# Kernel optimization log

Hardware: AMD Instinct MI355X
Metric: run time of the kernel (lower is better)

## Reference

```python
import jax, jax.numpy as jnp
import numpy as np

DIM = 256
NUM_HEADS = 8
HEAD_DIM = DIM // NUM_HEADS


def setup_inputs() -> dict:
    key = jax.random.key(0)
    k_x, k_wq, k_bq, k_wp, k_bp = jax.random.split(key, 5)
    B, C, H, W = 2, DIM, 48, 48
    x = jax.random.normal(k_x, (B, C, H, W), dtype=jnp.float32)
    # 1x1 convs are pointwise matmuls: store weights as [out, in]
    w_qkv = jax.random.normal(k_wq, (3 * C, C), dtype=jnp.float32) * (1.0 / np.sqrt(C))
    b_qkv = jax.random.normal(k_bq, (3 * C,), dtype=jnp.float32) * 0.01
    w_proj = jax.random.normal(k_wp, (C, C), dtype=jnp.float32) * (1.0 / np.sqrt(C))
    b_proj = jax.random.normal(k_bp, (C,), dtype=jnp.float32) * 0.01
    return {"x": x, "w_qkv": w_qkv, "b_qkv": b_qkv, "w_proj": w_proj, "b_proj": b_proj}


def reference(x, w_qkv, b_qkv, w_proj, b_proj):
    B, C, H, W = x.shape
    N = H * W
    # qkv 1x1 conv -> pointwise channel matmul
    qkv = jnp.einsum('bchw,oc->bohw', x, w_qkv) + b_qkv[None, :, None, None]
    q, k, v = jnp.split(qkv, 3, axis=1)  # each [B, C, H, W]
    q = q.reshape(B, NUM_HEADS, HEAD_DIM, N)
    k = k.reshape(B, NUM_HEADS, HEAD_DIM, N)
    v = v.reshape(B, NUM_HEADS, HEAD_DIM, N)
    scale = 1.0 / (HEAD_DIM ** 0.5)
    attn = jnp.einsum('bhdn,bhdm->bhnm', q, k) * scale  # [B, H, N, N]
    attn = jax.nn.softmax(attn, axis=-1)
    out = jnp.einsum('bhnm,bhdm->bhdn', attn, v)  # [B, heads, head_dim, N]
    out = out.reshape(B, C, H, W)
    out = jnp.einsum('bchw,oc->bohw', out, w_proj) + b_proj[None, :, None, None]
    return out + x
```

## Files before the change

### kernel.cpp

```cpp
#include <hip/hip_runtime.h>
#include <math.h>

#define C_DIM 256
#define NH 8
#define HD 32
#define BATCH 2
#define NPIX 2304
#define TK 64
#define NGRP (NPIX / 16)
#define TPB 36

typedef __attribute__((ext_vector_type(8))) short bf16x8;
typedef __attribute__((ext_vector_type(4))) float f32x4;

#define OFF_XT  0u
#define OFF_Q   1179648u
#define OFF_K   2359296u
#define OFF_V   3538944u
#define OFF_OT  4718592u
#define OFF_WQ  5898240u
#define OFF_WP  6094848u

__device__ __forceinline__ unsigned short f2b(float f) {
    union { float f; unsigned int u; } c; c.f = f;
    unsigned int u = c.u + 0x7FFFu + ((c.u >> 16) & 1u);
    return (unsigned short)(u >> 16);
}
__device__ __forceinline__ unsigned int pk2(float lo, float hi) {
    union { float f; unsigned int u; } a, b;
    a.f = lo; b.f = hi;
    return __builtin_amdgcn_perm(b.u + 0x8000u, a.u + 0x8000u, 0x07060302u);
}
__device__ __forceinline__ unsigned int cvtpk(float lo, float hi) {
    unsigned int r;
    asm("v_cvt_pk_bf16_f32 %0, %1, %2" : "=v"(r) : "v"(lo), "v"(hi));
    return r;
}
__device__ __forceinline__ float fexp2(float x) {
#if __has_builtin(__builtin_amdgcn_exp2f)
    return __builtin_amdgcn_exp2f(x);
#else
    return exp2f(x);
#endif
}

__global__ __launch_bounds__(256) void prep_all(
        const float* __restrict__ x, unsigned short* __restrict__ xT,
        const float* __restrict__ wqkv, const float* __restrict__ wproj,
        unsigned short* __restrict__ wq, unsigned short* __restrict__ wp)
{
    __shared__ unsigned short t_s[64][72];
    const int bid = blockIdx.x;
    const int tid = threadIdx.x;
    if (bid < 288) {
        const int bx = bid % 36, by = (bid / 36) & 3, bz = bid / 144;
        const int n0 = bx * 64, c0 = by * 64, b = bz;
        const int nl = tid & 63, cq = tid >> 6;
        #pragma unroll
        for (int p = 0; p < 8; ++p) {
            const int c = p * 8 + cq * 2;
            const float f0 = x[((size_t)b * C_DIM + c0 + c) * NPIX + n0 + nl];
            const float f1 = x[((size_t)b * C_DIM + c0 + c + 1) * NPIX + n0 + nl];
            *(unsigned int*)&t_s[nl][c] = pk2(f0, f1);
        }
        __syncthreads();
        const int row = tid >> 2, jq = tid & 3;
        #pragma unroll
        for (int hh = 0; hh < 2; ++hh) {
            const int jl = jq * 2 + hh;
            const int jg = by * 8 + jl;
            const int ngrp = bx * 4 + (row >> 4);
            unsigned short* dst = xT + (((size_t)b * NGRP + ngrp) * 32 + jg) * 128 + (row & 15) * 8;
            *(uint4*)dst = *(uint4*)&t_s[row][jl * 8];
        }
    } else {
        const int t = (bid - 288) * 256 + tid;
        const float* src; unsigned short* dst;
        if (t < 24576) {
            const int m = t >> 5, j = t & 31;
            src = wqkv + ((size_t)m * C_DIM + j * 8);
            dst = wq + ((size_t)((m >> 4) * 32 + j) * 16 + (m & 15)) * 8;
        } else {
            const int t2 = t - 24576, m = t2 >> 5, j = t2 & 31;
            src = wproj + ((size_t)m * C_DIM + j * 8);
            dst = wp + ((size_t)((m >> 4) * 32 + j) * 16 + (m & 15)) * 8;
        }
        const float4 f0 = *(const float4*)src, f1 = *(const float4*)(src + 4);
        *(uint4*)dst = make_uint4(pk2(f0.x, f0.y), pk2(f0.z, f0.w),
                                  pk2(f1.x, f1.y), pk2(f1.z, f1.w));
    }
}

__global__ __launch_bounds__(256, 2) void qkv_gemm(
        const unsigned short* __restrict__ xT, const unsigned short* __restrict__ wq,
        const float* __restrict__ bias,
        unsigned short* __restrict__ Qg, unsigned short* __restrict__ Kg,
        unsigned short* __restrict__ Vg)
{
    __shared__ unsigned short eplds[4][2560];
    const int tid = threadIdx.x, wv = tid >> 6, lane = tid & 63;
    const int l15 = lane & 15, quad = lane >> 4;
    const int n0 = blockIdx.x * 256, my = blockIdx.y, b = blockIdx.z;
    const int nw = n0 + wv * 64;

    bf16x8 af[2][8];
    #pragma unroll
    for (int mt = 0; mt < 2; ++mt)
        #pragma unroll
        for (int kc = 0; kc < 8; ++kc)
            af[mt][kc] = *(const bf16x8*)(wq +
                ((size_t)((my * 2 + mt) * 32 + kc * 4 + quad) * 16 + l15) * 8);

    f32x4 acc[2][4];
    #pragma unroll
    for (int mt = 0; mt < 2; ++mt)
        #pragma unroll
        for (int s = 0; s < 4; ++s) acc[mt][s] = (f32x4){0.f, 0.f, 0.f, 0.f};

    #pragma unroll
    for (int sub = 0; sub < 4; ++sub) {
        const int ngrp = (nw + sub * 16) >> 4;
        const unsigned short* bp = xT + ((size_t)b * NGRP + ngrp) * 32 * 128;
        #pragma unroll
        for (int kc = 0; kc < 8; ++kc) {
            const bf16x8 bf = *(const bf16x8*)(bp + (size_t)(kc * 4 + quad) * 128 + l15 * 8);
            acc[0][sub] = __builtin_amdgcn_mfma_f32_16x16x32_bf16(af[0][kc], bf, acc[0][sub], 0, 0, 0);
            acc[1][sub] = __builtin_amdgcn_mfma_f32_16x16x32_bf16(af[1][kc], bf, acc[1][sub], 0, 0, 0);
        }
    }

    const int which = my >> 3;
    const int h = my & 7, bh = b * NH + h;
    float4 b4[2];
    b4[0] = *(const float4*)(bias + my * 32 + quad * 4);
    b4[1] = *(const float4*)(bias + my * 32 + 16 + quad * 4);
    unsigned short* wl = eplds[wv];

    if (which < 2) {
        const float sc = (which == 0) ? 0.2550348576f : 1.0f;
        #pragma unroll
        for (int mt = 0; mt < 2; ++mt)
            #pragma unroll
            for (int sub = 0; sub < 4; ++sub) {
                const float v0 = (acc[mt][sub][0] + b4[mt].x) * sc;
                const float v1 = (acc[mt][sub][1] + b4[mt].y) * sc;
                const float v2 = (acc[mt][sub][2] + b4[mt].z) * sc;
                const float v3 = (acc[mt][sub][3] + b4[mt].w) * sc;
                *(uint2*)&wl[(sub * 16 + l15) * 40 + mt * 16 + quad * 4] =
                    make_uint2(pk2(v0, v1), pk2(v2, v3));
            }
        unsigned short* dst = ((which == 0) ? Qg : Kg)
                            + ((size_t)bh * NPIX + nw + lane) * HD;
        #pragma unroll
        for (int i = 0; i < 4; ++i)
            *((uint4*)dst + i) = *(uint4*)&wl[lane * 40 + i * 8];
    } else {
        #pragma unroll
        for (int mt = 0; mt < 2; ++mt)
            #pragma unroll
            for (int sub = 0; sub < 4; ++sub) {
                wl[(mt * 16 + quad * 4 + 0) * 72 + sub * 16 + l15] = f2b(acc[mt][sub][0] + b4[mt].x);
                wl[(mt * 16 + quad * 4 + 1) * 72 + sub * 16 + l15] = f2b(acc[mt][sub][1] + b4[mt].y);
                wl[(mt * 16 + quad * 4 + 2) * 72 + sub * 16 + l15] = f2b(acc[mt][sub][2] + b4[mt].z);
                wl[(mt * 16 + quad * 4 + 3) * 72 + sub * 16 + l15] = f2b(acc[mt][sub][3] + b4[mt].w);
            }
        const int row = lane >> 1, seg = (lane & 1) * 32;
        unsigned short* dst = Vg + ((size_t)bh * HD + row) * NPIX + nw + seg;
        #pragma unroll
        for (int i = 0; i < 4; ++i)
            *((uint4*)dst + i) = *(uint4*)&wl[row * 72 + seg + i * 8];
    }
}

__global__ __launch_bounds__(256, 4) void attn_kernel(
        const unsigned short* __restrict__ Qg, const unsigned short* __restrict__ Kg,
        const unsigned short* __restrict__ Vg,
        unsigned short* __restrict__ OtT)
{
    __shared__ unsigned short k_s[2][TK][40];
    __shared__ unsigned short v_s[2][HD][76];

    const int tid  = threadIdx.x;
    const int wv   = tid >> 6;
    const int lane = tid & 63;
    const int l15  = lane & 15;
    const int quad = lane >> 4;
    const int bh   = blockIdx.x;
    const int q0   = blockIdx.y * 64;

    const unsigned short* Qh = Qg + (size_t)bh * NPIX * HD;
    const unsigned short* Kh = Kg + (size_t)bh * NPIX * HD;
    const unsigned short* Vh = Vg + (size_t)bh * HD * NPIX;

    const bf16x8 q_frag = *(const bf16x8*)(Qh + (size_t)(q0 + wv * 16 + l15) * HD + quad * 8);
    const bf16x8 onesf = {16256, 16256, 16256, 16256, 16256, 16256, 16256, 16256};

    const int kr = tid >> 2, kc = (tid & 3) * 8;
    const int ksl = (kr & 0x23) | ((kr & 0x04) << 2) | ((kr & 0x18) >> 1);
    const int vd = tid >> 3, vc = (tid & 7) * 8;

    uint4 kreg = *(const uint4*)(Kh + (size_t)kr * HD + kc);
    uint4 vreg = *(const uint4*)(Vh + (size_t)vd * NPIX + vc);
    *(uint4*)&k_s[0][ksl][kc] = kreg;
    *(uint4*)&v_s[0][vd][vc] = vreg;

    f32x4 o0 = {0.f, 0.f, 0.f, 0.f};
    f32x4 o1 = {0.f, 0.f, 0.f, 0.f};
    f32x4 ol = {0.f, 0.f, 0.f, 0.f};

    for (int t = 0; t < TPB; ++t) {
        const int cur = t & 1;
        if (t + 1 < TPB) {
            const int k0 = (t + 1) * TK;
            kreg = *(const uint4*)(Kh + (size_t)(k0 + kr) * HD + kc);
            vreg = *(const uint4*)(Vh + (size_t)vd * NPIX + k0 + vc);
        }
        __syncthreads();

        f32x4 s[4];
        #pragma unroll
        for (int kg = 0; kg < 4; ++kg) {
            const bf16x8 kf = *(const bf16x8*)&k_s[cur][kg * 16 + l15][quad * 8];
            s[kg] = __builtin_amdgcn_mfma_f32_16x16x32_bf16(kf, q_frag,
                        (f32x4){0.f, 0.f, 0.f, 0.f}, 0, 0, 0);
        }

        bf16x8 pf[2];
        #pragma unroll
        for (int kc2 = 0; kc2 < 2; ++kc2) {
            union { unsigned int u[4]; bf16x8 v; } c;
            c.u[0] = cvtpk(fexp2(s[2 * kc2][0]),     fexp2(s[2 * kc2][1]));
            c.u[1] = cvtpk(fexp2(s[2 * kc2][2]),     fexp2(s[2 * kc2][3]));
            c.u[2] = cvtpk(fexp2(s[2 * kc2 + 1][0]), fexp2(s[2 * kc2 + 1][1]));
            c.u[3] = cvtpk(fexp2(s[2 * kc2 + 1][2]), fexp2(s[2 * kc2 + 1][3]));
            pf[kc2] = c.v;
        }

        #pragma unroll
        for (int kc2 = 0; kc2 < 2; ++kc2) {
            const bf16x8 vf0 = *(const bf16x8*)&v_s[cur][l15][kc2 * 32 + quad * 8];
            const bf16x8 vf1 = *(const bf16x8*)&v_s[cur][16 + l15][kc2 * 32 + quad * 8];
            o0 = __builtin_amdgcn_mfma_f32_16x16x32_bf16(vf0, pf[kc2], o0, 0, 0, 0);
            o1 = __builtin_amdgcn_mfma_f32_16x16x32_bf16(vf1, pf[kc2], o1, 0, 0, 0);
            ol = __builtin_amdgcn_mfma_f32_16x16x32_bf16(onesf, pf[kc2], ol, 0, 0, 0);
        }

        if (t + 1 < TPB) {
            *(uint4*)&k_s[cur ^ 1][ksl][kc] = kreg;
            *(uint4*)&v_s[cur ^ 1][vd][vc] = vreg;
        }
    }

    const float inv = 1.f / ol[0];
    const int b = bh >> 3, h = bh & 7;
    const int qg = q0 + wv * 16 + l15;
    unsigned short* base = OtT + (((size_t)b * NGRP + (qg >> 4)) * 32 + h * 4) * 128
                         + (qg & 15) * 8;
    const int jq0 = quad >> 1, half = (quad & 1) * 4;
    const uint2 w0 = make_uint2(cvtpk(o0[0] * inv, o0[1] * inv),
                                cvtpk(o0[2] * inv, o0[3] * inv));
    const uint2 w1 = make_uint2(cvtpk(o1[0] * inv, o1[1] * inv),
                                cvtpk(o1[2] * inv, o1[3] * inv));
    *(uint2*)(base + (size_t)jq0 * 128 + half)       = w0;
    *(uint2*)(base + (size_t)(2 + jq0) * 128 + half) = w1;
}

__global__ __launch_bounds__(256) void proj_gemm(
        const unsigned short* __restrict__ OtT, const unsigned short* __restrict__ wp,
        const float* __restrict__ bias, const float* __restrict__ x,
        float* __restrict__ out)
{
    __shared__ float plds[4][576];
    const int tid = threadIdx.x, wv = tid >> 6, lane = tid & 63;
    const int l15 = lane & 15, quad = lane >> 4;
    const int n0 = blockIdx.x * 128, my = blockIdx.y, b = blockIdx.z;
    const int nw = n0 + wv * 32;

    bf16x8 af[8];
    #pragma unroll
    for (int kc = 0; kc < 8; ++kc)
        af[kc] = *(const bf16x8*)(wp + ((size_t)(my * 32 + kc * 4 + quad) * 16 + l15) * 8);

    f32x4 acc[2];
    acc[0] = (f32x4){0.f, 0.f, 0.f, 0.f};
    acc[1] = (f32x4){0.f, 0.f, 0.f, 0.f};

    #pragma unroll
    for (int sub = 0; sub < 2; ++sub) {
        const int ngrp = (nw + sub * 16) >> 4;
        const unsigned short* bp = OtT + ((size_t)b * NGRP + ngrp) * 32 * 128;
        #pragma unroll
        for (int kc = 0; kc < 8; ++kc) {
            const bf16x8 bf = *(const bf16x8*)(bp + (size_t)(kc * 4 + quad) * 128 + l15 * 8);
            acc[sub] = __builtin_amdgcn_mfma_f32_16x16x32_bf16(af[kc], bf, acc[sub], 0, 0, 0);
        }
    }

    float* wl = plds[wv];
    #pragma unroll
    for (int sub = 0; sub < 2; ++sub) {
        wl[(quad * 4 + 0) * 36 + sub * 16 + l15] = acc[sub][0];
        wl[(quad * 4 + 1) * 36 + sub * 16 + l15] = acc[sub][1];
        wl[(quad * 4 + 2) * 36 + sub * 16 + l15] = acc[sub][2];
        wl[(quad * 4 + 3) * 36 + sub * 16 + l15] = acc[sub][3];
    }
    const int m0 = my * 16;
    #pragma unroll
    for (int p = 0; p < 2; ++p) {
        const int row = p * 8 + (lane >> 3), cn = (lane & 7) * 4;
        const int c = m0 + row;
        const size_t idx = ((size_t)b * C_DIM + c) * NPIX + nw + cn;
        const f32x4 v = *(const f32x4*)&wl[row * 36 + cn];
        const f32x4 r = *(const f32x4*)(x + idx);
        const float bv = bias[c];
        f32x4 o;
        o[0] = v[0] + bv + r[0]; o[1] = v[1] + bv + r[1];
        o[2] = v[2] + bv + r[2]; o[3] = v[3] + bv + r[3];
        *(f32x4*)(out + idx) = o;
    }
}

extern "C" void kernel_launch(void* const* d_in, const int* in_sizes, int n_in,
                              void* d_out, int out_size, void* d_ws, size_t ws_size,
                              hipStream_t stream)
{
    const float* x      = (const float*)d_in[0];
    const float* w_qkv  = (const float*)d_in[1];
    const float* b_qkv  = (const float*)d_in[2];
    const float* w_proj = (const float*)d_in[3];
    const float* b_proj = (const float*)d_in[4];
    float* out = (float*)d_out;

    unsigned short* ws = (unsigned short*)d_ws;
    unsigned short* xT  = ws + OFF_XT;
    unsigned short* Qg  = ws + OFF_Q;
    unsigned short* Kg  = ws + OFF_K;
    unsigned short* Vg  = ws + OFF_V;
    unsigned short* OtT = ws + OFF_OT;
    unsigned short* wq  = ws + OFF_WQ;
    unsigned short* wp  = ws + OFF_WP;

    prep_all<<<dim3(416), 256, 0, stream>>>(x, xT, w_qkv, w_proj, wq, wp);
    qkv_gemm<<<dim3(9, 24, 2), 256, 0, stream>>>(xT, wq, b_qkv, Qg, Kg, Vg);
    attn_kernel<<<dim3(16, 36), 256, 0, stream>>>(Qg, Kg, Vg, OtT);
    proj_gemm<<<dim3(18, 16, 2), 256, 0, stream>>>(OtT, wp, b_proj, x, out);
}
```

Baseline: 105.9 us.

## Fuse four kernels into one persistent kernel with global atomic barriers

Merges prep, QKV GEMM, attention and projection into one 576-block kernel, with a software grid barrier between stages built on an atomic counter and sleep-polling. A memset clears the counters on every call. The goal is to remove three kernel launch gaps and tail bubbles. The cost is barrier overhead and stages forced onto a fixed 576-block grid. Correctness depends on all blocks being co-resident, and the bounded spin guard could let a block through early if some blocks are not yet resident.

```diff
diff --git a/kernel.cpp b/kernel.cpp
--- a/kernel.cpp
+++ b/kernel.cpp
@@ -9,6 +9,7 @@
 #define TK 64
 #define NGRP (NPIX / 16)
 #define TPB 36
+#define NBLK 576
 
 typedef __attribute__((ext_vector_type(8))) short bf16x8;
 typedef __attribute__((ext_vector_type(4))) float f32x4;
@@ -20,6 +21,7 @@
 #define OFF_OT  4718592u
 #define OFF_WQ  5898240u
 #define OFF_WP  6094848u
+#define OFF_BAR 6160384u
 
 __device__ __forceinline__ unsigned short f2b(float f) {
     union { float f; unsigned int u; } c; c.f = f;
@@ -44,17 +46,40 @@
 #endif
 }
 
-__global__ __launch_bounds__(256) void prep_all(
+__device__ __forceinline__ void gbar(unsigned int* cnt) {
+    __syncthreads();
+    if (threadIdx.x == 0) {
+        __threadfence();
+        atomicAdd(cnt, 1u);
+        int guard = 0;
+        while (__hip_atomic_load(cnt, __ATOMIC_RELAXED, __HIP_MEMORY_SCOPE_AGENT)
+                   < (unsigned)NBLK && guard < (1 << 20)) {
+            __builtin_amdgcn_s_sleep(8);
+            ++guard;
+        }
+    }
+    __syncthreads();
+    __threadfence();
+}
+
+__global__ __launch_bounds__(256, 3) void fused_pipeline(
         const float* __restrict__ x, unsigned short* __restrict__ xT,
         const float* __restrict__ wqkv, const float* __restrict__ wproj,
-        unsigned short* __restrict__ wq, unsigned short* __restrict__ wp)
+        unsigned short* __restrict__ wq, unsigned short* __restrict__ wp,
+        const float* __restrict__ bqkv,
+        unsigned short* __restrict__ Qg, unsigned short* __restrict__ Kg,
+        unsigned short* __restrict__ Vg, unsigned short* __restrict__ OtT,
+        const float* __restrict__ bproj, float* __restrict__ out,
+        unsigned int* __restrict__ bar)
 {
-    __shared__ unsigned short t_s[64][72];
+    __shared__ __align__(16) unsigned char smem[20480];
     const int bid = blockIdx.x;
     const int tid = threadIdx.x;
+
     if (bid < 288) {
-        const int bx = bid % 36, by = (bid / 36) & 3, bz = bid / 144;
-        const int n0 = bx * 64, c0 = by * 64, b = bz;
+        unsigned short (*t_s)[72] = reinterpret_cast<unsigned short(*)[72]>(smem);
+        const int bx = bid % 36, by = (bid / 36) & 3, b = bid / 144;
+        const int n0 = bx * 64, c0 = by * 64;
         const int nl = tid & 63, cq = tid >> 6;
         #pragma unroll
         for (int p = 0; p < 8; ++p) {
@@ -73,7 +98,7 @@
             unsigned short* dst = xT + (((size_t)b * NGRP + ngrp) * 32 + jg) * 128 + (row & 15) * 8;
             *(uint4*)dst = *(uint4*)&t_s[row][jl * 8];
         }
-    } else {
+    } else if (bid < 416) {
         const int t = (bid - 288) * 256 + tid;
         const float* src; unsigned short* dst;
         if (t < 24576) {
@@ -89,234 +114,221 @@
         *(uint4*)dst = make_uint4(pk2(f0.x, f0.y), pk2(f0.z, f0.w),
                                   pk2(f1.x, f1.y), pk2(f1.z, f1.w));
     }
-}
-
-__global__ __launch_bounds__(256, 2) void qkv_gemm(
-        const unsigned short* __restrict__ xT, const unsigned short* __restrict__ wq,
-        const float* __restrict__ bias,
-        unsigned short* __restrict__ Qg, unsigned short* __restrict__ Kg,
-        unsigned short* __restrict__ Vg)
-{
-    __shared__ unsigned short eplds[4][2560];
-    const int tid = threadIdx.x, wv = tid >> 6, lane = tid & 63;
-    const int l15 = lane & 15, quad = lane >> 4;
-    const int n0 = blockIdx.x * 256, my = blockIdx.y, b = blockIdx.z;
-    const int nw = n0 + wv * 64;
-
-    bf16x8 af[2][8];
-    #pragma unroll
-    for (int mt = 0; mt < 2; ++mt)
+    gbar(bar + 0);
+
+    if (bid < 432) {
+        const int wv = tid >> 6, lane = tid & 63;
+        const int l15 = lane & 15, quad = lane >> 4;
+        const int bx = bid % 9, my = (bid / 9) % 24, b = bid / 216;
+        const int n0 = bx * 256;
+        const int nw = n0 + wv * 64;
+
+        bf16x8 af[2][8];
+        #pragma unroll
+        for (int mt = 0; mt < 2; ++mt)
+            #pragma unroll
+            for (int kc = 0; kc < 8; ++kc)
+                af[mt][kc] = *(const bf16x8*)(wq +
+                    ((size_t)((my * 2 + mt) * 32 + kc * 4 + quad) * 16 + l15) * 8);
+
+        f32x4 acc[2][4];
+        #pragma unroll
+        for (int mt = 0; mt < 2; ++mt)
+            #pragma unroll
+            for (int s = 0; s < 4; ++s) acc[mt][s] = (f32x4){0.f, 0.f, 0.f, 0.f};
+
+        #pragma unroll
+        for (int sub = 0; sub < 4; ++sub) {
+            const int ngrp = (nw + sub * 16) >> 4;
+            const unsigned short* bp = xT + ((size_t)b * NGRP + ngrp) * 32 * 128;
+            #pragma unroll
+            for (int kc = 0; kc < 8; ++kc) {
+                const bf16x8 bf = *(const bf16x8*)(bp + (size_t)(kc * 4 + quad) * 128 + l15 * 8);
+                acc[0][sub] = __builtin_amdgcn_mfma_f32_16x16x32_bf16(af[0][kc], bf, acc[0][sub], 0, 0, 0);
+                acc[1][sub] = __builtin_amdgcn_mfma_f32_16x16x32_bf16(af[1][kc], bf, acc[1][sub], 0, 0, 0);
+            }
+        }
+
+        const int which = my >> 3;
+        const int h = my & 7, bh = b * NH + h;
+        float4 b4[2];
+        b4[0] = *(const float4*)(bqkv + my * 32 + quad * 4);
+        b4[1] = *(const float4*)(bqkv + my * 32 + 16 + quad * 4);
+        unsigned short* wl = (unsigned short*)smem + wv * 2560;
+
+        if (which < 2) {
+            const float sc = (which == 0) ? 0.2550348576f : 1.0f;
+            #pragma unroll
+            for (int mt = 0; mt < 2; ++mt)
+                #pragma unroll
+                for (int sub = 0; sub < 4; ++sub) {
+                    const float v0 = (acc[mt][sub][0] + b4[mt].x) * sc;
+                    const float v1 = (acc[mt][sub][1] + b4[mt].y) * sc;
+                    const float v2 = (acc[mt][sub][2] + b4[mt].z) * sc;
+                    const float v3 = (acc[mt][sub][3] + b4[mt].w) * sc;
+                    *(uint2*)&wl[(sub * 16 + l15) * 40 + mt * 16 + quad * 4] =
+                        make_uint2(pk2(v0, v1), pk2(v2, v3));
+                }
+            unsigned short* dst = ((which == 0) ? Qg : Kg)
+                                + ((size_t)bh * NPIX + nw + lane) * HD;
+            #pragma unroll
+            for (int i = 0; i < 4; ++i)
+                *((uint4*)dst + i) = *(uint4*)&wl[lane * 40 + i * 8];
+        } else {
+            #pragma unroll
+            for (int mt = 0; mt < 2; ++mt)
+                #pragma unroll
+                for (int sub = 0; sub < 4; ++sub) {
+                    wl[(mt * 16 + quad * 4 + 0) * 72 + sub * 16 + l15] = f2b(acc[mt][sub][0] + b4[mt].x);
+                    wl[(mt * 16 + quad * 4 + 1) * 72 + sub * 16 + l15] = f2b(acc[mt][sub][1] + b4[mt].y);
+                    wl[(mt * 16 + quad * 4 + 2) * 72 + sub * 16 + l15] = f2b(acc[mt][sub][2] + b4[mt].z);
+                    wl[(mt * 16 + quad * 4 + 3) * 72 + sub * 16 + l15] = f2b(acc[mt][sub][3] + b4[mt].w);
+                }
+            const int row = lane >> 1, seg = (lane & 1) * 32;
+            unsigned short* dst = Vg + ((size_t)bh * HD + row) * NPIX + nw + seg;
+            #pragma unroll
+            for (int i = 0; i < 4; ++i)
+                *((uint4*)dst + i) = *(uint4*)&wl[row * 72 + seg + i * 8];
+        }
+    }
+    gbar(bar + 1);
+
+    {
+        unsigned short* ksb = (unsigned short*)smem;
+        unsigned short* vsb = (unsigned short*)smem + 5120;
+
+        const int wv = tid >> 6, lane = tid & 63;
+        const int l15 = lane & 15, quad = lane >> 4;
+        const int bh = bid & 15;
+        const int q0 = (bid >> 4) * 64;
+
+        const unsigned short* Qh = Qg + (size_t)bh * NPIX * HD;
+        const unsigned short* Kh = Kg + (size_t)bh * NPIX * HD;
+        const unsigned short* Vh = Vg + (size_t)bh * HD * NPIX;
+
+        const bf16x8 q_frag = *(const bf16x8*)(Qh + (size_t)(q0 + wv * 16 + l15) * HD + quad * 8);
+        const bf16x8 onesf = {16256, 16256, 16256, 16256, 16256, 16256, 16256, 16256};
+
+        const int kr = tid >> 2, kc = (tid & 3) * 8;
+        const int ksl = (kr & 0x23) | ((kr & 0x04) << 2) | ((kr & 0x18) >> 1);
+        const int vd = tid >> 3, vc = (tid & 7) * 8;
+
+        uint4 kreg = *(const uint4*)(Kh + (size_t)kr * HD + kc);
+        uint4 vreg = *(const uint4*)(Vh + (size_t)vd * NPIX + vc);
+        *(uint4*)(ksb + ksl * 40 + kc) = kreg;
+        *(uint4*)(vsb + vd * 76 + vc) = vreg;
+
+        f32x4 o0 = {0.f, 0.f, 0.f, 0.f};
+        f32x4 o1 = {0.f, 0.f, 0.f, 0.f};
+        f32x4 ol = {0.f, 0.f, 0.f, 0.f};
+
+        for (int t = 0; t < TPB; ++t) {
+            const int cur = t & 1;
+            if (t + 1 < TPB) {
+                const int k0 = (t + 1) * TK;
+                kreg = *(const uint4*)(Kh + (size_t)(k0 + kr) * HD + kc);
+                vreg = *(const uint4*)(Vh + (size_t)vd * NPIX + k0 + vc);
+            }
+            __syncthreads();
+
+            f32x4 s[4];
+            #pragma unroll
+            for (int kg = 0; kg < 4; ++kg) {
+                const bf16x8 kf = *(const bf16x8*)(ksb + cur * 2560 + (kg * 16 + l15) * 40 + quad * 8);
+                s[kg] = __builtin_amdgcn_mfma_f32_16x16x32_bf16(kf, q_frag,
+                            (f32x4){0.f, 0.f, 0.f, 0.f}, 0, 0, 0);
+            }
+
+            bf16x8 pf[2];
+            #pragma unroll
+            for (int kc2 = 0; kc2 < 2; ++kc2) {
+                union { unsigned int u[4]; bf16x8 v; } c;
+                c.u[0] = cvtpk(fexp2(s[2 * kc2][0]),     fexp2(s[2 * kc2][1]));
+                c.u[1] = cvtpk(fexp2(s[2 * kc2][2]),     fexp2(s[2 * kc2][3]));
+                c.u[2] = cvtpk(fexp2(s[2 * kc2 + 1][0]), fexp2(s[2 * kc2 + 1][1]));
+                c.u[3] = cvtpk(fexp2(s[2 * kc2 + 1][2]), fexp2(s[2 * kc2 + 1][3]));
+                pf[kc2] = c.v;
+            }
+
+            #pragma unroll
+            for (int kc2 = 0; kc2 < 2; ++kc2) {
+                const bf16x8 vf0 = *(const bf16x8*)(vsb + cur * 2432 + l15 * 76 + kc2 * 32 + quad * 8);
+                const bf16x8 vf1 = *(const bf16x8*)(vsb + cur * 2432 + (16 + l15) * 76 + kc2 * 32 + quad * 8);
+                o0 = __builtin_amdgcn_mfma_f32_16x16x32_bf16(vf0, pf[kc2], o0, 0, 0, 0);
+                o1 = __builtin_amdgcn_mfma_f32_16x16x32_bf16(vf1, pf[kc2], o1, 0, 0, 0);
+                ol = __builtin_amdgcn_mfma_f32_16x16x32_bf16(onesf, pf[kc2], ol, 0, 0, 0);
+            }
+
+            if (t + 1 < TPB) {
+                *(uint4*)(ksb + (cur ^ 1) * 2560 + ksl * 40 + kc) = kreg;
+                *(uint4*)(vsb + (cur ^ 1) * 2432 + vd * 76 + vc) = vreg;
+            }
+        }
+
+        const float inv = 1.f / ol[0];
+        const int b = bh >> 3, h = bh & 7;
+        const int qg = q0 + wv * 16 + l15;
+        unsigned short* base = OtT + (((size_t)b * NGRP + (qg >> 4)) * 32 + h * 4) * 128
+                             + (qg & 15) * 8;
+        const int jq0 = quad >> 1, half = (quad & 1) * 4;
+        const uint2 w0 = make_uint2(cvtpk(o0[0] * inv, o0[1] * inv),
+                                    cvtpk(o0[2] * inv, o0[3] * inv));
+        const uint2 w1 = make_uint2(cvtpk(o1[0] * inv, o1[1] * inv),
+                                    cvtpk(o1[2] * inv, o1[3] * inv));
+        *(uint2*)(base + (size_t)jq0 * 128 + half)       = w0;
+        *(uint2*)(base + (size_t)(2 + jq0) * 128 + half) = w1;
+    }
+    gbar(bar + 2);
+
+    {
+        const int wv = tid >> 6, lane = tid & 63;
+        const int l15 = lane & 15, quad = lane >> 4;
+        const int bx = bid % 18, my = (bid / 18) & 15, b = bid / 288;
+        const int n0 = bx * 128;
+        const int nw = n0 + wv * 32;
+
+        bf16x8 af[8];
         #pragma unroll
         for (int kc = 0; kc < 8; ++kc)
-            af[mt][kc] = *(const bf16x8*)(wq +
-                ((size_t)((my * 2 + mt) * 32 + kc * 4 + quad) * 16 + l15) * 8);
-
-    f32x4 acc[2][4];
-    #pragma unroll
-    for (int mt = 0; mt < 2; ++mt)
-        #pragma unroll
-        for (int s = 0; s < 4; ++s) acc[mt][s] = (f32x4){0.f, 0.f, 0.f, 0.f};
-
-    #pragma unroll
-    for (int sub = 0; sub < 4; ++sub) {
-        const int ngrp = (nw + sub * 16) >> 4;
-        const unsigned short* bp = xT + ((size_t)b * NGRP + ngrp) * 32 * 128;
-        #pragma unroll
-        for (int kc = 0; kc < 8; ++kc) {
-            const bf16x8 bf = *(const bf16x8*)(bp + (size_t)(kc * 4 + quad) * 128 + l15 * 8);
-            acc[0][sub] = __builtin_amdgcn_mfma_f32_16x16x32_bf16(af[0][kc], bf, acc[0][sub], 0, 0, 0);
-            acc[1][sub] = __builtin_amdgcn_mfma_f32_16x16x32_bf16(af[1][kc], bf, acc[1][sub], 0, 0, 0);
-        }
-    }
-
-    const int which = my >> 3;
-    const int h = my & 7, bh = b * NH + h;
-    float4 b4[2];
-    b4[0] = *(const float4*)(bias + my * 32 + quad * 4);
-    b4[1] = *(const float4*)(bias + my * 32 + 16 + quad * 4);
-    unsigned short* wl = eplds[wv];
-
-    if (which < 2) {
-        const float sc = (which == 0) ? 0.2550348576f : 1.0f;
-        #pragma unroll
-        for (int mt = 0; mt < 2; ++mt)
-            #pragma unroll
-            for (int sub = 0; sub < 4; ++sub) {
-                const float v0 = (acc[mt][sub][0] + b4[mt].x) * sc;
-                const float v1 = (acc[mt][sub][1] + b4[mt].y) * sc;
-                const float v2 = (acc[mt][sub][2] + b4[mt].z) * sc;
-                const float v3 = (acc[mt][sub][3] + b4[mt].w) * sc;
-                *(uint2*)&wl[(sub * 16 + l15) * 40 + mt * 16 + quad * 4] =
-                    make_uint2(pk2(v0, v1), pk2(v2, v3));
-            }
-        unsigned short* dst = ((which == 0) ? Qg : Kg)
-                            + ((size_t)bh * NPIX + nw + lane) * HD;
-        #pragma unroll
-        for (int i = 0; i < 4; ++i)
-            *((uint4*)dst + i) = *(uint4*)&wl[lane * 40 + i * 8];
-    } else {
-        #pragma unroll
-        for (int mt = 0; mt < 2; ++mt)
-            #pragma unroll
-            for (int sub = 0; sub < 4; ++sub) {
-                wl[(mt * 16 + quad * 4 + 0) * 72 + sub * 16 + l15] = f2b(acc[mt][sub][0] + b4[mt].x);
-                wl[(mt * 16 + quad * 4 + 1) * 72 + sub * 16 + l15] = f2b(acc[mt][sub][1] + b4[mt].y);
-                wl[(mt * 16 + quad * 4 + 2) * 72 + sub * 16 + l15] = f2b(acc[mt][sub][2] + b4[mt].z);
-                wl[(mt * 16 + quad * 4 + 3) * 72 + sub * 16 + l15] = f2b(acc[mt][sub][3] + b4[mt].w);
-            }
-        const int row = lane >> 1, seg = (lane & 1) * 32;
-        unsigned short* dst = Vg + ((size_t)bh * HD + row) * NPIX + nw + seg;
-        #pragma unroll
-        for (int i = 0; i < 4; ++i)
-            *((uint4*)dst + i) = *(uint4*)&wl[row * 72 + seg + i * 8];
-    }
-}
-
-__global__ __launch_bounds__(256, 4) void attn_kernel(
-        const unsigned short* __restrict__ Qg, const unsigned short* __restrict__ Kg,
-        const unsigned short* __restrict__ Vg,
-        unsigned short* __restrict__ OtT)
-{
-    __shared__ unsigned short k_s[2][TK][40];
-    __shared__ unsigned short v_s[2][HD][76];
-
-    const int tid  = threadIdx.x;
-    const int wv   = tid >> 6;
-    const int lane = tid & 63;
-    const int l15  = lane & 15;
-    const int quad = lane >> 4;
-    const int bh   = blockIdx.x;
-    const int q0   = blockIdx.y * 64;
-
-    const unsigned short* Qh = Qg + (size_t)bh * NPIX * HD;
-    const unsigned short* Kh = Kg + (size_t)bh * NPIX * HD;
-    const unsigned short* Vh = Vg + (size_t)bh * HD * NPIX;
-
-    const bf16x8 q_frag = *(const bf16x8*)(Qh + (size_t)(q0 + wv * 16 + l15) * HD + quad * 8);
-    const bf16x8 onesf = {16256, 16256, 16256, 16256, 16256, 16256, 16256, 16256};
-
-    const int kr = tid >> 2, kc = (tid & 3) * 8;
-    const int ksl = (kr & 0x23) | ((kr & 0x04) << 2) | ((kr & 0x18) >> 1);
-    const int vd = tid >> 3, vc = (tid & 7) * 8;
-
-    uint4 kreg = *(const uint4*)(Kh + (size_t)kr * HD + kc);
-    uint4 vreg = *(const uint4*)(Vh + (size_t)vd * NPIX + vc);
-    *(uint4*)&k_s[0][ksl][kc] = kreg;
-    *(uint4*)&v_s[0][vd][vc] = vreg;
-
-    f32x4 o0 = {0.f, 0.f, 0.f, 0.f};
-    f32x4 o1 = {0.f, 0.f, 0.f, 0.f};
-    f32x4 ol = {0.f, 0.f, 0.f, 0.f};
-
-    for (int t = 0; t < TPB; ++t) {
-        const int cur = t & 1;
-        if (t + 1 < TPB) {
-            const int k0 = (t + 1) * TK;
-            kreg = *(const uint4*)(Kh + (size_t)(k0 + kr) * HD + kc);
-            vreg = *(const uint4*)(Vh + (size_t)vd * NPIX + k0 + vc);
-        }
-        __syncthreads();
-
-        f32x4 s[4];
-        #pragma unroll
-        for (int kg = 0; kg < 4; ++kg) {
-            const bf16x8 kf = *(const bf16x8*)&k_s[cur][kg * 16 + l15][quad * 8];
-            s[kg] = __builtin_amdgcn_mfma_f32_16x16x32_bf16(kf, q_frag,
-                        (f32x4){0.f, 0.f, 0.f, 0.f}, 0, 0, 0);
-        }
-
-        bf16x8 pf[2];
-        #pragma unroll
-        for (int kc2 = 0; kc2 < 2; ++kc2) {
-            union { unsigned int u[4]; bf16x8 v; } c;
-            c.u[0] = cvtpk(fexp2(s[2 * kc2][0]),     fexp2(s[2 * kc2][1]));
-            c.u[1] = cvtpk(fexp2(s[2 * kc2][2]),     fexp2(s[2 * kc2][3]));
-            c.u[2] = cvtpk(fexp2(s[2 * kc2 + 1][0]), fexp2(s[2 * kc2 + 1][1]));
-            c.u[3] = cvtpk(fexp2(s[2 * kc2 + 1][2]), fexp2(s[2 * kc2 + 1][3]));
-            pf[kc2] = c.v;
-        }
-
-        #pragma unroll
-        for (int kc2 = 0; kc2 < 2; ++kc2) {
-            const bf16x8 vf0 = *(const bf16x8*)&v_s[cur][l15][kc2 * 32 + quad * 8];
-            const bf16x8 vf1 = *(const bf16x8*)&v_s[cur][16 + l15][kc2 * 32 + quad * 8];
-            o0 = __builtin_amdgcn_mfma_f32_16x16x32_bf16(vf0, pf[kc2], o0, 0, 0, 0);
-            o1 = __builtin_amdgcn_mfma_f32_16x16x32_bf16(vf1, pf[kc2], o1, 0, 0, 0);
-            ol = __builtin_amdgcn_mfma_f32_16x16x32_bf16(onesf, pf[kc2], ol, 0, 0, 0);
-        }
-
-        if (t + 1 < TPB) {
-            *(uint4*)&k_s[cur ^ 1][ksl][kc] = kreg;
-            *(uint4*)&v_s[cur ^ 1][vd][vc] = vreg;
-        }
-    }
-
-    const float inv = 1.f / ol[0];
-    const int b = bh >> 3, h = bh & 7;
-    const int qg = q0 + wv * 16 + l15;
-    unsigned short* base = OtT + (((size_t)b * NGRP + (qg >> 4)) * 32 + h * 4) * 128
-                         + (qg & 15) * 8;
-    const int jq0 = quad >> 1, half = (quad & 1) * 4;
-    const uint2 w0 = make_uint2(cvtpk(o0[0] * inv, o0[1] * inv),
-                                cvtpk(o0[2] * inv, o0[3] * inv));
-    const uint2 w1 = make_uint2(cvtpk(o1[0] * inv, o1[1] * inv),
-                                cvtpk(o1[2] * inv, o1[3] * inv));
-    *(uint2*)(base + (size_t)jq0 * 128 + half)       = w0;
-    *(uint2*)(base + (size_t)(2 + jq0) * 128 + half) = w1;
-}
-
-__global__ __launch_bounds__(256) void proj_gemm(
-        const unsigned short* __restrict__ OtT, const unsigned short* __restrict__ wp,
-        const float* __restrict__ bias, const float* __restrict__ x,
-        float* __restrict__ out)
-{
-    __shared__ float plds[4][576];
-    const int tid = threadIdx.x, wv = tid >> 6, lane = tid & 63;
-    const int l15 = lane & 15, quad = lane >> 4;
-    const int n0 = blockIdx.x * 128, my = blockIdx.y, b = blockIdx.z;
-    const int nw = n0 + wv * 32;
-
-    bf16x8 af[8];
-    #pragma unroll
-    for (int kc = 0; kc < 8; ++kc)
-        af[kc] = *(const bf16x8*)(wp + ((size_t)(my * 32 + kc * 4 + quad) * 16 + l15) * 8);
-
-    f32x4 acc[2];
-    acc[0] = (f32x4){0.f, 0.f, 0.f, 0.f};
-    acc[1] = (f32x4){0.f, 0.f, 0.f, 0.f};
-
-    #pragma unroll
-    for (int sub = 0; sub < 2; ++sub) {
-        const int ngrp = (nw + sub * 16) >> 4;
-        const unsigned short* bp = OtT + ((size_t)b * NGRP + ngrp) * 32 * 128;
-        #pragma unroll
-        for (int kc = 0; kc < 8; ++kc) {
-            const bf16x8 bf = *(const bf16x8*)(bp + (size_t)(kc * 4 + quad) * 128 + l15 * 8);
-            acc[sub] = __builtin_amdgcn_mfma_f32_16x16x32_bf16(af[kc], bf, acc[sub], 0, 0, 0);
-        }
-    }
-
-    float* wl = plds[wv];
-    #pragma unroll
-    for (int sub = 0; sub < 2; ++sub) {
-        wl[(quad * 4 + 0) * 36 + sub * 16 + l15] = acc[sub][0];
-        wl[(quad * 4 + 1) * 36 + sub * 16 + l15] = acc[sub][1];
-        wl[(quad * 4 + 2) * 36 + sub * 16 + l15] = acc[sub][2];
-        wl[(quad * 4 + 3) * 36 + sub * 16 + l15] = acc[sub][3];
-    }
-    const int m0 = my * 16;
-    #pragma unroll
-    for (int p = 0; p < 2; ++p) {
-        const int row = p * 8 + (lane >> 3), cn = (lane & 7) * 4;
-        const int c = m0 + row;
-        const size_t idx = ((size_t)b * C_DIM + c) * NPIX + nw + cn;
-        const f32x4 v = *(const f32x4*)&wl[row * 36 + cn];
-        const f32x4 r = *(const f32x4*)(x + idx);
-        const float bv = bias[c];
-        f32x4 o;
-        o[0] = v[0] + bv + r[0]; o[1] = v[1] + bv + r[1];
-        o[2] = v[2] + bv + r[2]; o[3] = v[3] + bv + r[3];
-        *(f32x4*)(out + idx) = o;
+            af[kc] = *(const bf16x8*)(wp + ((size_t)(my * 32 + kc * 4 + quad) * 16 + l15) * 8);
+
+        f32x4 acc[2];
+        acc[0] = (f32x4){0.f, 0.f, 0.f, 0.f};
+        acc[1] = (f32x4){0.f, 0.f, 0.f, 0.f};
+
+        #pragma unroll
+        for (int sub = 0; sub < 2; ++sub) {
+            const int ngrp = (nw + sub * 16) >> 4;
+            const unsigned short* bp = OtT + ((size_t)b * NGRP + ngrp) * 32 * 128;
+            #pragma unroll
+            for (int kc = 0; kc < 8; ++kc) {
+                const bf16x8 bf = *(const bf16x8*)(bp + (size_t)(kc * 4 + quad) * 128 + l15 * 8);
+                acc[sub] = __builtin_amdgcn_mfma_f32_16x16x32_bf16(af[kc], bf, acc[sub], 0, 0, 0);
+            }
+        }
+
+        float* wl = (float*)smem + wv * 576;
+        #pragma unroll
+        for (int sub = 0; sub < 2; ++sub) {
+            wl[(quad * 4 + 0) * 36 + sub * 16 + l15] = acc[sub][0];
+            wl[(quad * 4 + 1) * 36 + sub * 16 + l15] = acc[sub][1];
+            wl[(quad * 4 + 2) * 36 + sub * 16 + l15] = acc[sub][2];
+            wl[(quad * 4 + 3) * 36 + sub * 16 + l15] = acc[sub][3];
+        }
+        const int m0 = my * 16;
+        #pragma unroll
+        for (int p = 0; p < 2; ++p) {
+            const int row = p * 8 + (lane >> 3), cn = (lane & 7) * 4;
+            const int c = m0 + row;
+            const size_t idx = ((size_t)b * C_DIM + c) * NPIX + nw + cn;
+            const f32x4 v = *(const f32x4*)&wl[row * 36 + cn];
+            const f32x4 r = *(const f32x4*)(x + idx);
+            const float bv = bproj[c];
+            f32x4 o;
+            o[0] = v[0] + bv + r[0]; o[1] = v[1] + bv + r[1];
+            o[2] = v[2] + bv + r[2]; o[3] = v[3] + bv + r[3];
+            *(f32x4*)(out + idx) = o;
+        }
     }
 }
 
@@ -339,9 +351,10 @@
     unsigned short* OtT = ws + OFF_OT;
     unsigned short* wq  = ws + OFF_WQ;
     unsigned short* wp  = ws + OFF_WP;
-
-    prep_all<<<dim3(416), 256, 0, stream>>>(x, xT, w_qkv, w_proj, wq, wp);
-    qkv_gemm<<<dim3(9, 24, 2), 256, 0, stream>>>(xT, wq, b_qkv, Qg, Kg, Vg);
-    attn_kernel<<<dim3(16, 36), 256, 0, stream>>>(Qg, Kg, Vg, OtT);
-    proj_gemm<<<dim3(18, 16, 2), 256, 0, stream>>>(OtT, wp, b_proj, x, out);
-}
+    unsigned int* bar   = (unsigned int*)(ws + OFF_BAR);
+
+    hipMemsetAsync(bar, 0, 64, stream);
+    fused_pipeline<<<dim3(NBLK), 256, 0, stream>>>(
+        x, xT, w_qkv, w_proj, wq, wp, b_qkv,
+        Qg, Kg, Vg, OtT, b_proj, out, bar);
+}
```

Measured after the change: 399.5 us. +277.3%, slower.
